# Optimization experiments

Hardware: AMD Instinct MI355X
Metric: run time of the kernel (lower is better)

## Reference

```python
import jax, jax.numpy as jnp
import numpy as np

N_HEAD = 16

def setup_inputs() -> dict:
    key = jax.random.key(0)
    k1, k2, k3, k4, k5 = jax.random.split(key, 5)
    B, T, C = 2, 2048, 1024
    scale = 1.0 / np.sqrt(C)
    return {
        "x": jax.random.normal(k1, (B, T, C), dtype=jnp.float32),
        "Wqkv": jax.random.normal(k2, (C, 3 * C), dtype=jnp.float32) * scale,
        "bqkv": jax.random.normal(k3, (3 * C,), dtype=jnp.float32) * 0.02,
        "Wproj": jax.random.normal(k4, (C, C), dtype=jnp.float32) * scale,
        "bproj": jax.random.normal(k5, (C,), dtype=jnp.float32) * 0.02,
    }

def reference(x, Wqkv, bqkv, Wproj, bproj):
    B, T, C = x.shape
    H = N_HEAD
    D = C // H
    # qkv projection, split last dim as (3, H, D): first C cols = q, etc.
    qkv = (x @ Wqkv + bqkv).reshape(B, T, 3, H, D)
    q, k, v = qkv[:, :, 0], qkv[:, :, 1], qkv[:, :, 2]  # (B, T, H, D)
    att = jnp.einsum("bqhd,bkhd->bhqk", q, k) * (1.0 / np.sqrt(D))
    causal = jnp.tril(jnp.ones((T, T), dtype=bool))
    att = jnp.where(causal, att, -jnp.inf)
    att = jax.nn.softmax(att, axis=-1)
    y = jnp.einsum("bhqk,bkhd->bqhd", att, v).reshape(B, T, C)
    return y @ Wproj + bproj
```

## Files before the change

kernel.cpp:

```cpp
#include <hip/hip_runtime.h>
#include <hip/hip_bf16.h>
#include <stdint.h>

typedef unsigned short u16;
typedef __attribute__((ext_vector_type(8))) short bf16x8;
typedef __attribute__((ext_vector_type(4))) float f32x4;

#define MFMA16(a,b,c) __builtin_amdgcn_mfma_f32_16x16x32_bf16((a),(b),(c),0,0,0)

__device__ __forceinline__ u16 f2bf(float f) {
    union { float f; uint32_t u; } v; v.f = f;
    return (u16)((v.u + 0x7FFFu + ((v.u >> 16) & 1u)) >> 16);
}

__global__ void k_convert(const float* __restrict__ in, u16* __restrict__ out) {
    int i = (blockIdx.x * 256 + threadIdx.x) * 4;
    f32x4 v = *(const f32x4*)(in + i);
    uint64_t p = (uint64_t)f2bf(v[0]) | ((uint64_t)f2bf(v[1]) << 16)
               | ((uint64_t)f2bf(v[2]) << 32) | ((uint64_t)f2bf(v[3]) << 48);
    *(uint64_t*)(out + i) = p;
}

__global__ void k_transpose_convert(const float* __restrict__ W, u16* __restrict__ WT,
                                    int R, int NC) {
    int id = blockIdx.x * 256 + threadIdx.x;
    int n = id % NC, kc = id / NC;
    bf16x8 o;
#pragma unroll
    for (int i = 0; i < 8; ++i)
        o[i] = (short)f2bf(W[(size_t)(kc * 8 + i) * NC + n]);
    *(bf16x8*)(WT + (size_t)n * R + kc * 8) = o;
}

__global__ void k_transpose_v(const u16* __restrict__ V, u16* __restrict__ Vt) {
    int id = blockIdx.x * 256 + threadIdx.x;
    int d = id & 63, tc = (id >> 6) & 255, bh = id >> 14;
    const u16* src = V + (size_t)bh * 131072 + d;
    u16* dst = Vt + (size_t)bh * 131072 + (size_t)d * 2048 + tc * 8;
    bf16x8 o;
#pragma unroll
    for (int i = 0; i < 8; ++i) o[i] = (short)src[(size_t)(tc * 8 + i) * 64];
    *(bf16x8*)dst = o;
}

template<int NREP, int MODE>
__device__ __forceinline__ void gemm_body(
    const u16* __restrict__ A, const u16* __restrict__ Bt,
    const float* __restrict__ bias,
    u16* __restrict__ outQKV, float* __restrict__ outF,
    int M, int N, int K)
{
    constexpr int BN = 32 * NREP;
    constexpr int WN = 16 * NREP;
    constexpr int BSLOTS = NREP / 2;
    __shared__ __align__(16) u16 As[3][128 * 32];
    __shared__ __align__(16) u16 Bs[3][BN * 32];
    const int tid = threadIdx.x;
    const int nbx = N / BN;
    const int bm = blockIdx.x / nbx, bn = blockIdx.x % nbx;
    const int m0 = bm << 7, n0 = bn * BN;
    const int l = tid & 63, w = tid >> 6;
    const int wr = w >> 1, wc = w & 1;
    const int kl = l >> 4, lr = l & 15;

    const u16* Ag = A + (size_t)m0 * K;
    const u16* Bg = Bt + (size_t)n0 * K;

    int a_src[2], a_dst[2];
#pragma unroll
    for (int s = 0; s < 2; ++s) {
        int cb = w * 128 + s * 64;
        int c = cb + l;
        int r = c >> 2, kc = c & 3;
        a_src[s] = r * K + ((kc ^ ((r >> 1) & 3)) << 3);
        a_dst[s] = cb << 3;
    }
    int b_src[BSLOTS], b_dst[BSLOTS];
#pragma unroll
    for (int s = 0; s < BSLOTS; ++s) {
        int cb = (w * BSLOTS + s) * 64;
        int c = cb + l;
        int r = c >> 2, kc = c & 3;
        b_src[s] = r * K + ((kc ^ ((r >> 1) & 3)) << 3);
        b_dst[s] = cb << 3;
    }

    int ra[4], rb[NREP];
#pragma unroll
    for (int m = 0; m < 4; ++m) {
        int row = wr * 64 + m * 16 + lr;
        ra[m] = row * 32 + (((kl ^ (row >> 1)) & 3) << 3);
    }
#pragma unroll
    for (int n = 0; n < NREP; ++n) {
        int row = wc * WN + n * 16 + lr;
        rb[n] = row * 32 + (((kl ^ (row >> 1)) & 3) << 3);
    }

    f32x4 acc[4][NREP] = {};

    auto STAGE = [&](int buf, int koff) {
#pragma unroll
        for (int s = 0; s < 2; ++s)
            __builtin_amdgcn_global_load_lds(Ag + a_src[s] + koff,
                                             &As[buf][a_dst[s]], 16, 0, 0);
#pragma unroll
        for (int s = 0; s < BSLOTS; ++s)
            __builtin_amdgcn_global_load_lds(Bg + b_src[s] + koff,
                                             &Bs[buf][b_dst[s]], 16, 0, 0);
    };

    STAGE(0, 0);
    STAGE(1, 32);
    if constexpr (NREP == 4) asm volatile("s_waitcnt vmcnt(4)" ::: "memory");
    else                     asm volatile("s_waitcnt vmcnt(3)" ::: "memory");
    __builtin_amdgcn_s_barrier();
    __builtin_amdgcn_sched_barrier(0);

    const int nK = K >> 5;
    int rd = 0;
    for (int ks = 0; ks < nK; ++ks) {
        const bool st = (ks + 2 < nK);
        if (st) {
            int sb = rd + 2; if (sb >= 3) sb -= 3;
            STAGE(sb, (ks + 2) << 5);
        }
        bf16x8 af[4], bfr[NREP];
#pragma unroll
        for (int m = 0; m < 4; ++m) af[m] = *(const bf16x8*)&As[rd][ra[m]];
#pragma unroll
        for (int n = 0; n < NREP; ++n) bfr[n] = *(const bf16x8*)&Bs[rd][rb[n]];
#pragma unroll
        for (int m = 0; m < 4; ++m)
#pragma unroll
            for (int n = 0; n < NREP; ++n)
                acc[m][n] = MFMA16(af[m], bfr[n], acc[m][n]);
        if (ks + 1 < nK) {
            if (st) {
                if constexpr (NREP == 4) asm volatile("s_waitcnt vmcnt(4)" ::: "memory");
                else                     asm volatile("s_waitcnt vmcnt(3)" ::: "memory");
            } else {
                asm volatile("s_waitcnt vmcnt(0)" ::: "memory");
            }
            __builtin_amdgcn_s_barrier();
            __builtin_amdgcn_sched_barrier(0);
        }
        rd = (rd == 2) ? 0 : rd + 1;
    }

    if (MODE == 0) {
#pragma unroll
        for (int n = 0; n < NREP; ++n) {
            int gn = n0 + wc * WN + n * 16 + lr;
            float bv = bias[gn];
            int s = gn >> 10, hd = gn & 1023;
            int hh = hd >> 6, dd = hd & 63;
            float mult = (s == 0) ? 0.125f : 1.0f;
            size_t base = (size_t)s * 4194304 + (size_t)hh * 131072 + dd;
#pragma unroll
            for (int m = 0; m < 4; ++m)
#pragma unroll
                for (int j = 0; j < 4; ++j) {
                    int gm = m0 + wr * 64 + m * 16 + kl * 4 + j;
                    int bb = gm >> 11, tt = gm & 2047;
                    float val = (acc[m][n][j] + bv) * mult;
                    outQKV[base + (size_t)bb * 2097152 + (size_t)tt * 64] = f2bf(val);
                }
        }
    } else {
#pragma unroll
        for (int n = 0; n < NREP; ++n) {
            int gn = n0 + wc * WN + n * 16 + lr;
            float bv = bias[gn];
#pragma unroll
            for (int m = 0; m < 4; ++m)
#pragma unroll
                for (int j = 0; j < 4; ++j) {
                    int gm = m0 + wr * 64 + m * 16 + kl * 4 + j;
                    outF[(size_t)gm * N + gn] = acc[m][n][j] + bv;
                }
        }
    }
}

__global__ __launch_bounds__(256, 3) void k_gemm_qkv(
    const u16* __restrict__ A, const u16* __restrict__ Bt,
    const float* __restrict__ bias, u16* __restrict__ outQKV,
    int M, int N, int K)
{
    gemm_body<4, 0>(A, Bt, bias, outQKV, nullptr, M, N, K);
}

__global__ __launch_bounds__(256, 3) void k_gemm_proj(
    const u16* __restrict__ A, const u16* __restrict__ Bt,
    const float* __restrict__ bias, float* __restrict__ outF,
    int M, int N, int K)
{
    gemm_body<2, 1>(A, Bt, bias, nullptr, outF, M, N, K);
}

__global__ __launch_bounds__(256, 4) void k_attn(
    const u16* __restrict__ Qg, const u16* __restrict__ Kg,
    const u16* __restrict__ Vtg, u16* __restrict__ Yg)
{
    const int bid = blockIdx.x;
    const int bh = bid & 31;
    const int qt = 31 - (bid >> 5);
    const int b = bh >> 4, h = bh & 15;
    const int q0 = qt << 6;
    const int tid = threadIdx.x, l = tid & 63, w = tid >> 6;
    const int kl = l >> 4, lr = l & 15;

    __shared__ __align__(16) u16 Qs[64 * 64];
    __shared__ __align__(16) u16 Ks[64 * 64];
    __shared__ __align__(16) u16 Vs[64 * 64];
    __shared__ __align__(16) u16 Ps[4][16 * 72];

    const u16* Qb = Qg + (size_t)bh * 131072;
    const u16* Kb = Kg + (size_t)bh * 131072;
    const u16* Vb = Vtg + (size_t)bh * 131072;

    const int rr = tid >> 3, ch = tid & 7;
    {
        bf16x8 a = *(const bf16x8*)(Qb + (size_t)(q0 + rr) * 64 + ch * 8);
        bf16x8 c = *(const bf16x8*)(Qb + (size_t)(q0 + rr + 32) * 64 + ch * 8);
        *(bf16x8*)&Qs[rr * 64 + ((ch ^ (rr & 7)) << 3)] = a;
        *(bf16x8*)&Qs[(rr + 32) * 64 + ((ch ^ (rr & 7)) << 3)] = c;
    }
    __syncthreads();
    bf16x8 qa[2];
#pragma unroll
    for (int kk = 0; kk < 2; ++kk) {
        int row = w * 16 + lr;
        qa[kk] = *(const bf16x8*)&Qs[row * 64 + (((kk * 4 + kl) ^ (row & 7)) << 3)];
    }

    f32x4 oacc[4] = {};
    float lsum[4] = {0.f, 0.f, 0.f, 0.f};

    bf16x8 kv0 = *(const bf16x8*)(Kb + (size_t)rr * 64 + ch * 8);
    bf16x8 kv1 = *(const bf16x8*)(Kb + (size_t)(rr + 32) * 64 + ch * 8);
    bf16x8 vv0 = *(const bf16x8*)(Vb + (size_t)rr * 2048 + ch * 8);
    bf16x8 vv1 = *(const bf16x8*)(Vb + (size_t)(rr + 32) * 2048 + ch * 8);

    for (int kt = 0; kt <= qt; ++kt) {
        const int k0 = kt << 6;
        __syncthreads();
        *(bf16x8*)&Ks[rr * 64 + ((ch ^ (rr & 7)) << 3)] = kv0;
        *(bf16x8*)&Ks[(rr + 32) * 64 + ((ch ^ (rr & 7)) << 3)] = kv1;
        *(bf16x8*)&Vs[rr * 64 + ((ch ^ (rr & 7)) << 3)] = vv0;
        *(bf16x8*)&Vs[(rr + 32) * 64 + ((ch ^ (rr & 7)) << 3)] = vv1;
        __syncthreads();
        if (kt < qt) {
            const int k0n = k0 + 64;
            kv0 = *(const bf16x8*)(Kb + (size_t)(k0n + rr) * 64 + ch * 8);
            kv1 = *(const bf16x8*)(Kb + (size_t)(k0n + rr + 32) * 64 + ch * 8);
            vv0 = *(const bf16x8*)(Vb + (size_t)rr * 2048 + k0n + ch * 8);
            vv1 = *(const bf16x8*)(Vb + (size_t)(rr + 32) * 2048 + k0n + ch * 8);
        }

        f32x4 s[4];
#pragma unroll
        for (int nb = 0; nb < 4; ++nb) {
            f32x4 a = {};
            int key = nb * 16 + lr;
#pragma unroll
            for (int kk = 0; kk < 2; ++kk) {
                bf16x8 kb = *(const bf16x8*)&Ks[key * 64 + (((kk * 4 + kl) ^ (key & 7)) << 3)];
                a = MFMA16(qa[kk], kb, a);
            }
            s[nb] = a;
        }
        if (kt == qt) {
#pragma unroll
            for (int nb = 0; nb < 4; ++nb) {
                int key = k0 + nb * 16 + lr;
#pragma unroll
                for (int j = 0; j < 4; ++j) {
                    int q = q0 + w * 16 + kl * 4 + j;
                    if (key > q) s[nb][j] = -__builtin_inff();
                }
            }
        }
#pragma unroll
        for (int j = 0; j < 4; ++j) {
            float acc4 = 0.f;
#pragma unroll
            for (int nb = 0; nb < 4; ++nb) {
                float p = __expf(s[nb][j]);
                s[nb][j] = p;
                acc4 += p;
            }
            lsum[j] += acc4;
        }
#pragma unroll
        for (int nb = 0; nb < 4; ++nb)
#pragma unroll
            for (int j = 0; j < 4; ++j)
                Ps[w][(kl * 4 + j) * 72 + nb * 16 + lr] = f2bf(s[nb][j]);
        bf16x8 pa[2];
#pragma unroll
        for (int kk = 0; kk < 2; ++kk)
            pa[kk] = *(const bf16x8*)&Ps[w][lr * 72 + kk * 32 + kl * 8];
#pragma unroll
        for (int db = 0; db < 4; ++db) {
            int d = db * 16 + lr;
#pragma unroll
            for (int kk = 0; kk < 2; ++kk) {
                bf16x8 vb = *(const bf16x8*)&Vs[d * 64 + (((kk * 4 + kl) ^ (d & 7)) << 3)];
                oacc[db] = MFMA16(pa[kk], vb, oacc[db]);
            }
        }
    }
#pragma unroll
    for (int j = 0; j < 4; ++j) {
#pragma unroll
        for (int off = 1; off < 16; off <<= 1) lsum[j] += __shfl_xor(lsum[j], off);
        lsum[j] = 1.f / lsum[j];
    }
#pragma unroll
    for (int db = 0; db < 4; ++db)
#pragma unroll
        for (int j = 0; j < 4; ++j) {
            int q = q0 + w * 16 + kl * 4 + j;
            int col = h * 64 + db * 16 + lr;
            Yg[(size_t)(b * 2048 + q) * 1024 + col] = f2bf(oacc[db][j] * lsum[j]);
        }
}

extern "C" void kernel_launch(void* const* d_in, const int* in_sizes, int n_in,
                              void* d_out, int out_size, void* d_ws, size_t ws_size,
                              hipStream_t stream) {
    const float* x     = (const float*)d_in[0];
    const float* Wqkv  = (const float*)d_in[1];
    const float* bqkv  = (const float*)d_in[2];
    const float* Wproj = (const float*)d_in[3];
    const float* bproj = (const float*)d_in[4];
    float* out = (float*)d_out;

    char* ws = (char*)d_ws;
    u16* xb     = (u16*)(ws);
    u16* WqkvT  = (u16*)(ws + 8388608);
    u16* WprojT = (u16*)(ws + 14680064);
    u16* qkv    = (u16*)(ws + 16777216);
    u16* Vt   = xb;
    u16* Yatt = qkv + 2 * 4194304;

    k_convert<<<4096, 256, 0, stream>>>(x, xb);
    k_transpose_convert<<<1536, 256, 0, stream>>>(Wqkv, WqkvT, 1024, 3072);
    k_transpose_convert<<<512, 256, 0, stream>>>(Wproj, WprojT, 1024, 1024);
    k_gemm_qkv<<<768, 256, 0, stream>>>(xb, WqkvT, bqkv, qkv,
                                        4096, 3072, 1024);
    k_transpose_v<<<2048, 256, 0, stream>>>(qkv + 2 * 4194304, Vt);
    k_attn<<<1024, 256, 0, stream>>>(qkv, qkv + 4194304, Vt, Yatt);
    k_gemm_proj<<<512, 256, 0, stream>>>(Yatt, WprojT, bproj, out,
                                         4096, 1024, 1024);
}
```

Measured before the change: 121.4 us.

## Use dedicated 256x256-tile QKV GEMM kernel with 512 threads

Replaces the templated 128x128 QKV GEMM with a standalone kernel using 256x256 output tiles, 8 waves per block, and 8x4 MFMA accumulators per wave, launched as 192 blocks of 512 threads. Larger tiles raise arithmetic intensity per LDS load and cut global traffic for the QKV projection. The trade-off is fewer blocks (192 on a 256-CU part, so under one wave of work), higher register and LDS pressure, and possible load imbalance. The generic body is simplified to the projection-only path.

After: 133.4 us. 1.1x slower.

```diff
diff --git a/kernel.cpp b/kernel.cpp
--- a/kernel.cpp
+++ b/kernel.cpp
@@ -41,6 +41,111 @@
 #pragma unroll
     for (int i = 0; i < 8; ++i) o[i] = (short)src[(size_t)(tc * 8 + i) * 64];
     *(bf16x8*)dst = o;
+}
+
+__global__ __launch_bounds__(512, 2) void k_gemm_qkv(
+    const u16* __restrict__ A, const u16* __restrict__ Bt,
+    const float* __restrict__ bias, u16* __restrict__ outQKV,
+    int M, int N, int K)
+{
+    __shared__ __align__(16) u16 As[3][256 * 32];
+    __shared__ __align__(16) u16 Bs[3][256 * 32];
+    const int tid = threadIdx.x;
+    const int nbx = N >> 8;
+    const int bm = blockIdx.x / nbx, bn = blockIdx.x % nbx;
+    const int m0 = bm << 8, n0 = bn << 8;
+    const int l = tid & 63, w = tid >> 6;
+    const int wr = w >> 2, wc = w & 3;
+    const int kl = l >> 4, lr = l & 15;
+
+    const u16* Ag = A + (size_t)m0 * K;
+    const u16* Bg = Bt + (size_t)n0 * K;
+
+    int g_src[2], g_dst[2];
+#pragma unroll
+    for (int s = 0; s < 2; ++s) {
+        int cb = (w * 2 + s) * 64;
+        int c = cb + l;
+        int r = c >> 2, kc = c & 3;
+        g_src[s] = r * K + ((kc ^ ((r >> 1) & 3)) << 3);
+        g_dst[s] = cb << 3;
+    }
+
+    int ra[8], rb[4];
+#pragma unroll
+    for (int m = 0; m < 8; ++m) {
+        int row = wr * 128 + m * 16 + lr;
+        ra[m] = row * 32 + (((kl ^ (row >> 1)) & 3) << 3);
+    }
+#pragma unroll
+    for (int n = 0; n < 4; ++n) {
+        int row = wc * 64 + n * 16 + lr;
+        rb[n] = row * 32 + (((kl ^ (row >> 1)) & 3) << 3);
+    }
+
+    f32x4 acc[8][4] = {};
+
+    auto STAGE = [&](int buf, int koff) {
+#pragma unroll
+        for (int s = 0; s < 2; ++s) {
+            __builtin_amdgcn_global_load_lds(Ag + g_src[s] + koff,
+                                             &As[buf][g_dst[s]], 16, 0, 0);
+            __builtin_amdgcn_global_load_lds(Bg + g_src[s] + koff,
+                                             &Bs[buf][g_dst[s]], 16, 0, 0);
+        }
+    };
+
+    STAGE(0, 0);
+    STAGE(1, 32);
+    asm volatile("s_waitcnt vmcnt(4)" ::: "memory");
+    __builtin_amdgcn_s_barrier();
+    __builtin_amdgcn_sched_barrier(0);
+
+    const int nK = K >> 5;
+    int rd = 0;
+    for (int ks = 0; ks < nK; ++ks) {
+        const bool st = (ks + 2 < nK);
+        if (st) {
+            int sb = rd + 2; if (sb >= 3) sb -= 3;
+            STAGE(sb, (ks + 2) << 5);
+        }
+        bf16x8 af[8], bfr[4];
+#pragma unroll
+        for (int m = 0; m < 8; ++m) af[m] = *(const bf16x8*)&As[rd][ra[m]];
+#pragma unroll
+        for (int n = 0; n < 4; ++n) bfr[n] = *(const bf16x8*)&Bs[rd][rb[n]];
+#pragma unroll
+        for (int m = 0; m < 8; ++m)
+#pragma unroll
+            for (int n = 0; n < 4; ++n)
+                acc[m][n] = MFMA16(af[m], bfr[n], acc[m][n]);
+        if (ks + 1 < nK) {
+            if (st) asm volatile("s_waitcnt vmcnt(4)" ::: "memory");
+            else    asm volatile("s_waitcnt vmcnt(0)" ::: "memory");
+            __builtin_amdgcn_s_barrier();
+            __builtin_amdgcn_sched_barrier(0);
+        }
+        rd = (rd == 2) ? 0 : rd + 1;
+    }
+
+#pragma unroll
+    for (int n = 0; n < 4; ++n) {
+        int gn = n0 + wc * 64 + n * 16 + lr;
+        float bv = bias[gn];
+        int s = gn >> 10, hd = gn & 1023;
+        int hh = hd >> 6, dd = hd & 63;
+        float mult = (s == 0) ? 0.125f : 1.0f;
+        size_t base = (size_t)s * 4194304 + (size_t)hh * 131072 + dd;
+#pragma unroll
+        for (int m = 0; m < 8; ++m)
+#pragma unroll
+            for (int j = 0; j < 4; ++j) {
+                int gm = m0 + wr * 128 + m * 16 + kl * 4 + j;
+                int bb = gm >> 11, tt = gm & 2047;
+                float val = (acc[m][n][j] + bv) * mult;
+                outQKV[base + (size_t)bb * 2097152 + (size_t)tt * 64] = f2bf(val);
+            }
+    }
 }
 
 template<int NREP, int MODE>
@@ -112,8 +217,7 @@
 
     STAGE(0, 0);
     STAGE(1, 32);
-    if constexpr (NREP == 4) asm volatile("s_waitcnt vmcnt(4)" ::: "memory");
-    else                     asm volatile("s_waitcnt vmcnt(3)" ::: "memory");
+    asm volatile("s_waitcnt vmcnt(3)" ::: "memory");
     __builtin_amdgcn_s_barrier();
     __builtin_amdgcn_sched_barrier(0);
 
@@ -136,59 +240,26 @@
             for (int n = 0; n < NREP; ++n)
                 acc[m][n] = MFMA16(af[m], bfr[n], acc[m][n]);
         if (ks + 1 < nK) {
-            if (st) {
-                if constexpr (NREP == 4) asm volatile("s_waitcnt vmcnt(4)" ::: "memory");
-                else                     asm volatile("s_waitcnt vmcnt(3)" ::: "memory");
-            } else {
-                asm volatile("s_waitcnt vmcnt(0)" ::: "memory");
-            }
+            if (st) asm volatile("s_waitcnt vmcnt(3)" ::: "memory");
+            else    asm volatile("s_waitcnt vmcnt(0)" ::: "memory");
             __builtin_amdgcn_s_barrier();
             __builtin_amdgcn_sched_barrier(0);
         }
         rd = (rd == 2) ? 0 : rd + 1;
     }
 
-    if (MODE == 0) {
-#pragma unroll
-        for (int n = 0; n < NREP; ++n) {
-            int gn = n0 + wc * WN + n * 16 + lr;
-            float bv = bias[gn];
-            int s = gn >> 10, hd = gn & 1023;
-            int hh = hd >> 6, dd = hd & 63;
-            float mult = (s == 0) ? 0.125f : 1.0f;
-            size_t base = (size_t)s * 4194304 + (size_t)hh * 131072 + dd;
-#pragma unroll
-            for (int m = 0; m < 4; ++m)
-#pragma unroll
-                for (int j = 0; j < 4; ++j) {
-                    int gm = m0 + wr * 64 + m * 16 + kl * 4 + j;
-                    int bb = gm >> 11, tt = gm & 2047;
-                    float val = (acc[m][n][j] + bv) * mult;
-                    outQKV[base + (size_t)bb * 2097152 + (size_t)tt * 64] = f2bf(val);
-                }
-        }
-    } else {
-#pragma unroll
-        for (int n = 0; n < NREP; ++n) {
-            int gn = n0 + wc * WN + n * 16 + lr;
-            float bv = bias[gn];
-#pragma unroll
-            for (int m = 0; m < 4; ++m)
-#pragma unroll
-                for (int j = 0; j < 4; ++j) {
-                    int gm = m0 + wr * 64 + m * 16 + kl * 4 + j;
-                    outF[(size_t)gm * N + gn] = acc[m][n][j] + bv;
-                }
-        }
-    }
-}
-
-__global__ __launch_bounds__(256, 3) void k_gemm_qkv(
-    const u16* __restrict__ A, const u16* __restrict__ Bt,
-    const float* __restrict__ bias, u16* __restrict__ outQKV,
-    int M, int N, int K)
-{
-    gemm_body<4, 0>(A, Bt, bias, outQKV, nullptr, M, N, K);
+#pragma unroll
+    for (int n = 0; n < NREP; ++n) {
+        int gn = n0 + wc * WN + n * 16 + lr;
+        float bv = bias[gn];
+#pragma unroll
+        for (int m = 0; m < 4; ++m)
+#pragma unroll
+            for (int j = 0; j < 4; ++j) {
+                int gm = m0 + wr * 64 + m * 16 + kl * 4 + j;
+                outF[(size_t)gm * N + gn] = acc[m][n][j] + bv;
+            }
+    }
 }
 
 __global__ __launch_bounds__(256, 3) void k_gemm_proj(
@@ -349,7 +420,7 @@
     k_convert<<<4096, 256, 0, stream>>>(x, xb);
     k_transpose_convert<<<1536, 256, 0, stream>>>(Wqkv, WqkvT, 1024, 3072);
     k_transpose_convert<<<512, 256, 0, stream>>>(Wproj, WprojT, 1024, 1024);
-    k_gemm_qkv<<<768, 256, 0, stream>>>(xb, WqkvT, bqkv, qkv,
+    k_gemm_qkv<<<192, 512, 0, stream>>>(xb, WqkvT, bqkv, qkv,
                                         4096, 3072, 1024);
     k_transpose_v<<<2048, 256, 0, stream>>>(qkv + 2 * 4194304, Vt);
     k_attn<<<1024, 256, 0, stream>>>(qkv, qkv + 4194304, Vt, Yatt);
```

## Split-K the output projection GEMM with 128-wide tiles plus a bias-reduce pass

Applied to the files above, without the earlier changes.

Replaces the projection GEMM (128x64 tiles, 512 blocks) with a two-way split-K version using 128x128 tiles, so there are still 512 blocks but each tile reuses its loads better. Each split writes fp32 partial sums to workspace, and a separate kernel adds the two partials plus the bias. This trades extra global traffic (two 16 MB partial buffers written and read back) and one more kernel launch for better per-block data reuse. It falls back to the old kernel when the workspace is too small.

Result: slower. 127.2 us (+4.8%).

```diff
diff --git a/kernel.cpp b/kernel.cpp
--- a/kernel.cpp
+++ b/kernel.cpp
@@ -48,7 +48,7 @@
     const u16* __restrict__ A, const u16* __restrict__ Bt,
     const float* __restrict__ bias,
     u16* __restrict__ outQKV, float* __restrict__ outF,
-    int M, int N, int K)
+    int M, int N, int tileId, int Kstride, int Klen)
 {
     constexpr int BN = 32 * NREP;
     constexpr int WN = 16 * NREP;
@@ -57,14 +57,14 @@
     __shared__ __align__(16) u16 Bs[3][BN * 32];
     const int tid = threadIdx.x;
     const int nbx = N / BN;
-    const int bm = blockIdx.x / nbx, bn = blockIdx.x % nbx;
+    const int bm = tileId / nbx, bn = tileId % nbx;
     const int m0 = bm << 7, n0 = bn * BN;
     const int l = tid & 63, w = tid >> 6;
     const int wr = w >> 1, wc = w & 1;
     const int kl = l >> 4, lr = l & 15;
 
-    const u16* Ag = A + (size_t)m0 * K;
-    const u16* Bg = Bt + (size_t)n0 * K;
+    const u16* Ag = A + (size_t)m0 * Kstride;
+    const u16* Bg = Bt + (size_t)n0 * Kstride;
 
     int a_src[2], a_dst[2];
 #pragma unroll
@@ -72,7 +72,7 @@
         int cb = w * 128 + s * 64;
         int c = cb + l;
         int r = c >> 2, kc = c & 3;
-        a_src[s] = r * K + ((kc ^ ((r >> 1) & 3)) << 3);
+        a_src[s] = r * Kstride + ((kc ^ ((r >> 1) & 3)) << 3);
         a_dst[s] = cb << 3;
     }
     int b_src[BSLOTS], b_dst[BSLOTS];
@@ -81,7 +81,7 @@
         int cb = (w * BSLOTS + s) * 64;
         int c = cb + l;
         int r = c >> 2, kc = c & 3;
-        b_src[s] = r * K + ((kc ^ ((r >> 1) & 3)) << 3);
+        b_src[s] = r * Kstride + ((kc ^ ((r >> 1) & 3)) << 3);
         b_dst[s] = cb << 3;
     }
 
@@ -117,7 +117,7 @@
     __builtin_amdgcn_s_barrier();
     __builtin_amdgcn_sched_barrier(0);
 
-    const int nK = K >> 5;
+    const int nK = Klen >> 5;
     int rd = 0;
     for (int ks = 0; ks < nK; ++ks) {
         const bool st = (ks + 2 < nK);
@@ -167,7 +167,7 @@
                     outQKV[base + (size_t)bb * 2097152 + (size_t)tt * 64] = f2bf(val);
                 }
         }
-    } else {
+    } else if (MODE == 1) {
 #pragma unroll
         for (int n = 0; n < NREP; ++n) {
             int gn = n0 + wc * WN + n * 16 + lr;
@@ -180,6 +180,18 @@
                     outF[(size_t)gm * N + gn] = acc[m][n][j] + bv;
                 }
         }
+    } else {
+#pragma unroll
+        for (int n = 0; n < NREP; ++n) {
+            int gn = n0 + wc * WN + n * 16 + lr;
+#pragma unroll
+            for (int m = 0; m < 4; ++m)
+#pragma unroll
+                for (int j = 0; j < 4; ++j) {
+                    int gm = m0 + wr * 64 + m * 16 + kl * 4 + j;
+                    outF[(size_t)gm * N + gn] = acc[m][n][j];
+                }
+        }
     }
 }
 
@@ -188,7 +200,7 @@
     const float* __restrict__ bias, u16* __restrict__ outQKV,
     int M, int N, int K)
 {
-    gemm_body<4, 0>(A, Bt, bias, outQKV, nullptr, M, N, K);
+    gemm_body<4, 0>(A, Bt, bias, outQKV, nullptr, M, N, blockIdx.x, K, K);
 }
 
 __global__ __launch_bounds__(256, 3) void k_gemm_proj(
@@ -196,7 +208,33 @@
     const float* __restrict__ bias, float* __restrict__ outF,
     int M, int N, int K)
 {
-    gemm_body<2, 1>(A, Bt, bias, nullptr, outF, M, N, K);
+    gemm_body<2, 1>(A, Bt, bias, nullptr, outF, M, N, blockIdx.x, K, K);
+}
+
+__global__ __launch_bounds__(256, 3) void k_gemm_proj_split(
+    const u16* __restrict__ A, const u16* __restrict__ Bt,
+    float* __restrict__ partial, int M, int N, int K)
+{
+    const int nbt = (M >> 7) * (N >> 7);
+    const int split = blockIdx.x / nbt;
+    const int tile = blockIdx.x % nbt;
+    const int kh = K >> 1;
+    gemm_body<4, 2>(A + split * kh, Bt + split * kh, nullptr, nullptr,
+                    partial + (size_t)split * M * N, M, N, tile, K, kh);
+}
+
+__global__ void k_reduce_bias(const float* __restrict__ p,
+                              const float* __restrict__ bias,
+                              float* __restrict__ out, int total, int N)
+{
+    int i = (blockIdx.x * 256 + threadIdx.x) * 4;
+    f32x4 a = *(const f32x4*)(p + i);
+    f32x4 b = *(const f32x4*)(p + total + i);
+    f32x4 c = *(const f32x4*)(bias + (i & (N - 1)));
+    f32x4 r;
+#pragma unroll
+    for (int j = 0; j < 4; ++j) r[j] = a[j] + b[j] + c[j];
+    *(f32x4*)(out + i) = r;
 }
 
 __global__ __launch_bounds__(256, 4) void k_attn(
@@ -353,6 +391,17 @@
                                         4096, 3072, 1024);
     k_transpose_v<<<2048, 256, 0, stream>>>(qkv + 2 * 4194304, Vt);
     k_attn<<<1024, 256, 0, stream>>>(qkv, qkv + 4194304, Vt, Yatt);
-    k_gemm_proj<<<512, 256, 0, stream>>>(Yatt, WprojT, bproj, out,
-                                         4096, 1024, 1024);
-}
+
+    const size_t pbase = 41943040;
+    const size_t need  = pbase + 2u * 16777216;
+    if (ws_size >= need) {
+        float* partial = (float*)(ws + pbase);
+        k_gemm_proj_split<<<512, 256, 0, stream>>>(Yatt, WprojT, partial,
+                                                   4096, 1024, 1024);
+        k_reduce_bias<<<4096, 256, 0, stream>>>(partial, bproj, out,
+                                                4194304, 1024);
+    } else {
+        k_gemm_proj<<<512, 256, 0, stream>>>(Yatt, WprojT, bproj, out,
+                                             4096, 1024, 1024);
+    }
+}
```

## Fuse V transpose into QKV GEMM epilogue and remap GEMM tiles across XCDs

Applied to the files above, without the earlier changes.

The QKV GEMM epilogue now writes the V slice directly in transposed (d-major) layout using packed 64-bit stores, so the separate k_transpose_v kernel and its extra read and write pass over V are removed. Workspace buffers are reassigned so Vt lives in the qkv region and the attention output reuses the xb buffer. Both GEMMs also remap blockIdx so that consecutive tiles land on the same XCD (stride of 8), aiming for better L2 reuse of A and B panels. The transposed V stores stride by 2048 elements per lane, which may be less coalesced than before.

Result: faster. 113.5 us (-6.6%).

```diff
diff --git a/kernel.cpp b/kernel.cpp
--- a/kernel.cpp
+++ b/kernel.cpp
@@ -32,23 +32,12 @@
     *(bf16x8*)(WT + (size_t)n * R + kc * 8) = o;
 }
 
-__global__ void k_transpose_v(const u16* __restrict__ V, u16* __restrict__ Vt) {
-    int id = blockIdx.x * 256 + threadIdx.x;
-    int d = id & 63, tc = (id >> 6) & 255, bh = id >> 14;
-    const u16* src = V + (size_t)bh * 131072 + d;
-    u16* dst = Vt + (size_t)bh * 131072 + (size_t)d * 2048 + tc * 8;
-    bf16x8 o;
-#pragma unroll
-    for (int i = 0; i < 8; ++i) o[i] = (short)src[(size_t)(tc * 8 + i) * 64];
-    *(bf16x8*)dst = o;
-}
-
 template<int NREP, int MODE>
 __device__ __forceinline__ void gemm_body(
     const u16* __restrict__ A, const u16* __restrict__ Bt,
     const float* __restrict__ bias,
     u16* __restrict__ outQKV, float* __restrict__ outF,
-    int M, int N, int K)
+    int M, int N, int tileId, int K)
 {
     constexpr int BN = 32 * NREP;
     constexpr int WN = 16 * NREP;
@@ -57,7 +46,7 @@
     __shared__ __align__(16) u16 Bs[3][BN * 32];
     const int tid = threadIdx.x;
     const int nbx = N / BN;
-    const int bm = blockIdx.x / nbx, bn = blockIdx.x % nbx;
+    const int bm = tileId / nbx, bn = tileId % nbx;
     const int m0 = bm << 7, n0 = bn * BN;
     const int l = tid & 63, w = tid >> 6;
     const int wr = w >> 1, wc = w & 1;
@@ -155,17 +144,32 @@
             float bv = bias[gn];
             int s = gn >> 10, hd = gn & 1023;
             int hh = hd >> 6, dd = hd & 63;
-            float mult = (s == 0) ? 0.125f : 1.0f;
-            size_t base = (size_t)s * 4194304 + (size_t)hh * 131072 + dd;
-#pragma unroll
-            for (int m = 0; m < 4; ++m)
-#pragma unroll
-                for (int j = 0; j < 4; ++j) {
-                    int gm = m0 + wr * 64 + m * 16 + kl * 4 + j;
+            if (s == 2) {
+                size_t vb = (size_t)2 * 4194304 + (size_t)hh * 131072
+                          + (size_t)dd * 2048;
+#pragma unroll
+                for (int m = 0; m < 4; ++m) {
+                    int gm = m0 + wr * 64 + m * 16 + kl * 4;
                     int bb = gm >> 11, tt = gm & 2047;
-                    float val = (acc[m][n][j] + bv) * mult;
-                    outQKV[base + (size_t)bb * 2097152 + (size_t)tt * 64] = f2bf(val);
+                    uint64_t p = (uint64_t)f2bf(acc[m][n][0] + bv)
+                               | ((uint64_t)f2bf(acc[m][n][1] + bv) << 16)
+                               | ((uint64_t)f2bf(acc[m][n][2] + bv) << 32)
+                               | ((uint64_t)f2bf(acc[m][n][3] + bv) << 48);
+                    *(uint64_t*)(outQKV + vb + (size_t)bb * 2097152 + tt) = p;
                 }
+            } else {
+                float mult = (s == 0) ? 0.125f : 1.0f;
+                size_t base = (size_t)s * 4194304 + (size_t)hh * 131072 + dd;
+#pragma unroll
+                for (int m = 0; m < 4; ++m)
+#pragma unroll
+                    for (int j = 0; j < 4; ++j) {
+                        int gm = m0 + wr * 64 + m * 16 + kl * 4 + j;
+                        int bb = gm >> 11, tt = gm & 2047;
+                        float val = (acc[m][n][j] + bv) * mult;
+                        outQKV[base + (size_t)bb * 2097152 + (size_t)tt * 64] = f2bf(val);
+                    }
+            }
         }
     } else {
 #pragma unroll
@@ -188,7 +192,8 @@
     const float* __restrict__ bias, u16* __restrict__ outQKV,
     int M, int N, int K)
 {
-    gemm_body<4, 0>(A, Bt, bias, outQKV, nullptr, M, N, K);
+    int tile = (blockIdx.x & 7) * (gridDim.x >> 3) + (blockIdx.x >> 3);
+    gemm_body<4, 0>(A, Bt, bias, outQKV, nullptr, M, N, tile, K);
 }
 
 __global__ __launch_bounds__(256, 3) void k_gemm_proj(
@@ -196,7 +201,8 @@
     const float* __restrict__ bias, float* __restrict__ outF,
     int M, int N, int K)
 {
-    gemm_body<2, 1>(A, Bt, bias, nullptr, outF, M, N, K);
+    int tile = (blockIdx.x & 7) * (gridDim.x >> 3) + (blockIdx.x >> 3);
+    gemm_body<2, 1>(A, Bt, bias, nullptr, outF, M, N, tile, K);
 }
 
 __global__ __launch_bounds__(256, 4) void k_attn(
@@ -343,15 +349,14 @@
     u16* WqkvT  = (u16*)(ws + 8388608);
     u16* WprojT = (u16*)(ws + 14680064);
     u16* qkv    = (u16*)(ws + 16777216);
-    u16* Vt   = xb;
-    u16* Yatt = qkv + 2 * 4194304;
+    u16* Vt   = qkv + 2 * 4194304;
+    u16* Yatt = xb;
 
     k_convert<<<4096, 256, 0, stream>>>(x, xb);
     k_transpose_convert<<<1536, 256, 0, stream>>>(Wqkv, WqkvT, 1024, 3072);
     k_transpose_convert<<<512, 256, 0, stream>>>(Wproj, WprojT, 1024, 1024);
     k_gemm_qkv<<<768, 256, 0, stream>>>(xb, WqkvT, bqkv, qkv,
                                         4096, 3072, 1024);
-    k_transpose_v<<<2048, 256, 0, stream>>>(qkv + 2 * 4194304, Vt);
     k_attn<<<1024, 256, 0, stream>>>(qkv, qkv + 4194304, Vt, Yatt);
     k_gemm_proj<<<512, 256, 0, stream>>>(Yatt, WprojT, bproj, out,
                                          4096, 1024, 1024);
```
